# Performance work log

Measured on AMD Instinct MI355X. Metric: run time of the kernel, lower is better.

The kernel has to match this reference:

```python
import jax, jax.numpy as jnp
import numpy as np

B, S, H, NH, HD = 2, 1024, 1024, 16, 64
L, C, E, K, D = 256, 2048, 8, 2, 2048
EPS = 1e-5


def _ln(x):
    m = x.mean(-1, keepdims=True)
    v = x.var(-1, keepdims=True)
    return (x - m) * jax.lax.rsqrt(v + EPS)


def _rot_half(x):
    h = x.shape[-1] // 2
    return jnp.concatenate([-x[..., h:], x[..., :h]], axis=-1)


def _attn(q, k, v, scale):
    s = jnp.einsum('bhqd,bhkd->bhqk', q, k) * scale
    p = jax.nn.softmax(s, axis=-1)
    return jnp.einsum('bhqk,bhkd->bhqd', p, v)


def _forward(x, condition, enc, rope_cos, rope_sin, adaln_w, adaln_b, qw, qb, kw, kb, vw, vb, ow, ob, cqw, cqb, ckw, ckb, cvw, cvb, cow, cob, cn_g, cn_b, gate_w, ew1, eb1, ew2, eb2):
    b, s, hdim = x.shape
    # AdaLN-Zero modulation params (condition is per-sample vector)
    mod = jax.nn.silu(condition) @ adaln_w + adaln_b
    sh1, sc1, g1, sh2, sc2, g2 = jnp.split(mod, 6, axis=-1)
    # --- self-attention with RoPE ---
    h = _ln(x) * (1 + sc1[:, None]) + sh1[:, None]
    q = (h @ qw + qb).reshape(b, s, NH, HD).transpose(0, 2, 1, 3)
    k = (h @ kw + kb).reshape(b, s, NH, HD).transpose(0, 2, 1, 3)
    v = (h @ vw + vb).reshape(b, s, NH, HD).transpose(0, 2, 1, 3)
    cos = rope_cos[None, None]
    sin = rope_sin[None, None]
    q = q * cos + _rot_half(q) * sin
    k = k * cos + _rot_half(k) * sin
    a = _attn(q, k, v, 1.0 / np.sqrt(HD)).transpose(0, 2, 1, 3).reshape(b, s, hdim)
    x = x + g1[:, None] * (a @ ow + ob)
    # --- cross-attention (affine LayerNorm) ---
    hc = _ln(x) * cn_g + cn_b
    lq = (hc @ cqw + cqb).reshape(b, s, NH, HD).transpose(0, 2, 1, 3)
    lk = (enc @ ckw + ckb).reshape(b, -1, NH, HD).transpose(0, 2, 1, 3)
    lv = (enc @ cvw + cvb).reshape(b, -1, NH, HD).transpose(0, 2, 1, 3)
    ca = _attn(lq, lk, lv, 1.0 / np.sqrt(HD)).transpose(0, 2, 1, 3).reshape(b, s, hdim)
    x = x + ca @ cow + cob
    # --- MoE FFN with AdaLN-Zero modulation ---
    h = _ln(x) * (1 + sc2[:, None]) + sh2[:, None]
    logits = h @ gate_w                                   # [B,S,E]
    probs = jax.nn.softmax(logits, axis=-1)
    topp, topi = jax.lax.top_k(probs, K)                  # [B,S,K]
    topp = topp / topp.sum(-1, keepdims=True)
    onehot = jax.nn.one_hot(topi, E, dtype=x.dtype)       # [B,S,K,E]
    cw = (onehot * topp[..., None]).sum(-2)               # [B,S,E] combine weights
    tokens_per_expert = onehot.sum(-2).mean(0)            # [S,E] (matches torch one_hot(...).sum(-2).mean(0))
    avg_prob = probs.mean((0, 1))                         # [E]
    aux = E * (tokens_per_expert * avg_prob).sum()
    hf = h.reshape(-1, hdim)                              # [T,H]
    act = jax.nn.gelu(jnp.einsum('th,ehd->ted', hf, ew1) + eb1, approximate=False)
    y = jnp.einsum('ted,edh->teh', act, ew2) + eb2        # [T,E,H]
    moe = jnp.einsum('te,teh->th', cw.reshape(-1, E), y).reshape(b, s, hdim)
    x = x + g2[:, None] * moe
    return x, aux


def setup_inputs() -> dict:
    key = jax.random.key(0)
    ks = jax.random.split(key, 30)
    w = lambda i, shape: (jax.random.normal(ks[i], shape) * 0.02).astype(jnp.float32)
    pos = jnp.arange(S, dtype=jnp.float32)[:, None]
    inv = 1.0 / (10000.0 ** (jnp.arange(0, HD, 2, dtype=jnp.float32) / HD))
    ang = jnp.concatenate([pos * inv[None, :]] * 2, axis=-1)  # [S,HD]
    return dict(
        x=jax.random.normal(ks[0], (B, S, H), jnp.float32),
        condition=jax.random.normal(ks[1], (B, H), jnp.float32),
        enc=jax.random.normal(ks[2], (B, L, C), jnp.float32),
        rope_cos=jnp.cos(ang).astype(jnp.float32),
        rope_sin=jnp.sin(ang).astype(jnp.float32),
        adaln_w=w(3, (H, 6 * H)), adaln_b=w(4, (6 * H,)),
        qw=w(5, (H, H)), qb=w(6, (H,)), kw=w(7, (H, H)), kb=w(8, (H,)),
        vw=w(9, (H, H)), vb=w(10, (H,)), ow=w(11, (H, H)), ob=w(12, (H,)),
        cqw=w(13, (H, H)), cqb=w(14, (H,)), ckw=w(15, (C, H)), ckb=w(16, (H,)),
        cvw=w(17, (C, H)), cvb=w(18, (H,)), cow=w(19, (H, H)), cob=w(20, (H,)),
        cn_g=jnp.ones((H,), jnp.float32), cn_b=jnp.zeros((H,), jnp.float32),
        gate_w=w(21, (H, E)),
        ew1=w(22, (E, H, D)), eb1=w(23, (E, D)),
        ew2=w(24, (E, D, H)), eb2=w(25, (E, H)),
    )


def reference(x, condition, enc, rope_cos, rope_sin, adaln_w, adaln_b, qw, qb, kw, kb, vw, vb, ow, ob, cqw, cqb, ckw, ckb, cvw, cvb, cow, cob, cn_g, cn_b, gate_w, ew1, eb1, ew2, eb2):
    return _forward(x, condition, enc, rope_cos, rope_sin, adaln_w, adaln_b, qw, qb, kw, kb, vw, vb, ow, ob, cqw, cqb, ckw, ckb, cvw, cvb, cow, cob, cn_g, cn_b, gate_w, ew1, eb1, ew2, eb2)
```

## Files before the change

### kernel.cpp

```cpp
#include <hip/hip_runtime.h>
#include <math.h>

#define Hh 1024
#define Ss 1024
#define Bb 2
#define NHh 16
#define HDd 64
#define Tt 2048
#define Ll 256
#define Cc 2048
#define Ee 8
#define Dd 2048
#define EPSf 1e-5f
#define PADROWS 5120

using bf16x8 = __attribute__((ext_vector_type(8))) short;
using f32x4  = __attribute__((ext_vector_type(4))) float;
using ushort8 = __attribute__((ext_vector_type(8))) unsigned short;

__device__ __forceinline__ float geluf(float x) {
    return 0.5f * x * (1.0f + erff(x * 0.70710678118654752f));
}

__device__ __forceinline__ unsigned short f2bf(float x) {
    union { float f; unsigned int u; } c; c.f = x;
    unsigned int r = (c.u + 0x7fffu + ((c.u >> 16) & 1u)) >> 16;
    return (unsigned short)r;
}

__device__ __forceinline__ void gload16(const void* g, void* l) {
    __builtin_amdgcn_global_load_lds(
        (const __attribute__((address_space(1))) void*)g,
        (__attribute__((address_space(3))) void*)l, 16, 0, 0);
}

__device__ __forceinline__ void tcast_tile(const float* __restrict__ src,
        unsigned short* __restrict__ dst, int R, int C, int lt,
        unsigned short* __restrict__ tb, int tid) {
    int gx = R >> 7;
    int rt = lt % gx, ct = lt / gx;
    int r0 = rt * 128, c0 = ct * 64;
    int lr = tid >> 4;
    int lc4 = (tid & 15) << 2;
    #pragma unroll
    for (int p = 0; p < 8; ++p) {
        int row = lr + 16 * p;
        float4 v = *(const float4*)&src[(size_t)(r0 + row) * C + c0 + lc4];
        ushort4 h; h.x = f2bf(v.x); h.y = f2bf(v.y); h.z = f2bf(v.z); h.w = f2bf(v.w);
        *(ushort4*)&tb[row * 70 + lc4] = h;
    }
    __syncthreads();
    int wr = tid >> 5;
    int wc4 = (tid & 31) << 2;
    #pragma unroll
    for (int p = 0; p < 8; ++p) {
        int orow = wr + 8 * p;
        ushort4 o;
        o.x = tb[(wc4 + 0) * 70 + orow];
        o.y = tb[(wc4 + 1) * 70 + orow];
        o.z = tb[(wc4 + 2) * 70 + orow];
        o.w = tb[(wc4 + 3) * 70 + orow];
        *(ushort4*)&dst[(size_t)(c0 + orow) * R + r0 + wc4] = o;
    }
}

__global__ __launch_bounds__(256) void prep_all(
        const float* __restrict__ qw, const float* __restrict__ kw, const float* __restrict__ vw,
        const float* __restrict__ ow, const float* __restrict__ cqw, const float* __restrict__ cow,
        const float* __restrict__ ckw, const float* __restrict__ cvw,
        const float* __restrict__ enc,
        const float* __restrict__ qb, const float* __restrict__ kb, const float* __restrict__ vb,
        const float* __restrict__ ckb, const float* __restrict__ cvb,
        unsigned short* __restrict__ qkvwT, unsigned short* __restrict__ owT,
        unsigned short* __restrict__ cqwT, unsigned short* __restrict__ cowT,
        unsigned short* __restrict__ ckvwT, unsigned short* __restrict__ encb,
        float* __restrict__ qkvb, float* __restrict__ ckvb) {
    __shared__ unsigned short tb[128 * 70];
    int bid = blockIdx.x;
    int tid = threadIdx.x;
    const float* src;
    unsigned short* dst;
    int R, C, lt;
    if (bid < 768) {
        int seg = bid >> 7;
        lt = bid & 127;
        R = 1024; C = 1024;
        switch (seg) {
            case 0: src = qw;  dst = qkvwT; break;
            case 1: src = kw;  dst = qkvwT + (size_t)1024 * 1024; break;
            case 2: src = vw;  dst = qkvwT + (size_t)2048 * 1024; break;
            case 3: src = ow;  dst = owT; break;
            case 4: src = cqw; dst = cqwT; break;
            default: src = cow; dst = cowT; break;
        }
    } else if (bid < 1024) {
        lt = bid - 768; src = ckw; dst = ckvwT; R = 2048; C = 1024;
    } else if (bid < 1280) {
        lt = bid - 1024; src = cvw; dst = ckvwT + (size_t)1024 * 2048; R = 2048; C = 1024;
    } else if (bid < 2304) {
        int i = (bid - 1280) * 256 + tid;
        float4 v = ((const float4*)enc)[i];
        ushort4 o; o.x = f2bf(v.x); o.y = f2bf(v.y); o.z = f2bf(v.z); o.w = f2bf(v.w);
        ((ushort4*)encb)[i] = o;
        return;
    } else {
        int i = (bid - 2304) * 256 + tid;
        if (i < 1024) qkvb[i] = qb[i];
        else if (i < 2048) qkvb[i] = kb[i - 1024];
        else if (i < 3072) qkvb[i] = vb[i - 2048];
        else if (i < 4096) ckvb[i - 3072] = ckb[i - 3072];
        else if (i < 5120) ckvb[i - 3072] = cvb[i - 4096];
        return;
    }
    tcast_tile(src, dst, R, C, lt, tb, tid);
}

__global__ __launch_bounds__(256) void vtrans16(const unsigned short* __restrict__ in,
        unsigned short* __restrict__ out, int S) {
    __shared__ unsigned short sm[32][36];
    int bh = blockIdx.z;
    int s0 = blockIdx.x * 32, d0 = blockIdx.y * 32;
    int lr = threadIdx.x >> 3, lc = (threadIdx.x & 7) << 2;
    ushort4 v = *(const ushort4*)&in[((size_t)bh * S + s0 + lr) * 64 + d0 + lc];
    sm[lr][lc] = v.x; sm[lr][lc + 1] = v.y; sm[lr][lc + 2] = v.z; sm[lr][lc + 3] = v.w;
    __syncthreads();
    ushort4 o;
    o.x = sm[lc + 0][lr]; o.y = sm[lc + 1][lr]; o.z = sm[lc + 2][lr]; o.w = sm[lc + 3][lr];
    *(ushort4*)&out[((size_t)bh * 64 + d0 + lr) * S + s0 + lc] = o;
}

__global__ __launch_bounds__(256) void adaln_kernel(const float* __restrict__ cond,
        const float* __restrict__ w, const float* __restrict__ b, float* __restrict__ mod) {
    __shared__ float ss[Hh];
    int bi = (blockIdx.x * 256) / (6 * Hh);
    const float* cp = cond + (size_t)bi * Hh;
    for (int i = threadIdx.x; i < Hh; i += 256) {
        float c = cp[i];
        ss[i] = c / (1.0f + expf(-c));
    }
    __syncthreads();
    int idx = blockIdx.x * 256 + threadIdx.x;
    int j = idx % (6 * Hh);
    float acc = b[j];
    for (int i = 0; i < Hh; ++i) acc += ss[i] * w[(size_t)i * (6 * Hh) + j];
    mod[idx] = acc;
}

template<int OM>
__global__ __launch_bounds__(256) void ln_affine(const float* __restrict__ X, float* __restrict__ O32,
        unsigned short* __restrict__ O16,
        const float* __restrict__ scale, const float* __restrict__ shift, int bstride, float add1) {
    int t = blockIdx.x;
    int tid = threadIdx.x;
    const float* xr = X + (size_t)t * Hh;
    float4 xv = *(const float4*)&xr[tid * 4];
    float s = xv.x + xv.y + xv.z + xv.w;
    float q = xv.x * xv.x + xv.y * xv.y + xv.z * xv.z + xv.w * xv.w;
    #pragma unroll
    for (int off = 32; off > 0; off >>= 1) {
        s += __shfl_down(s, off);
        q += __shfl_down(q, off);
    }
    __shared__ float rsum[4], rsq[4];
    __shared__ float smean, srstd;
    int wv = tid >> 6, ln = tid & 63;
    if (ln == 0) { rsum[wv] = s; rsq[wv] = q; }
    __syncthreads();
    if (tid == 0) {
        float ts = rsum[0] + rsum[1] + rsum[2] + rsum[3];
        float tq = rsq[0] + rsq[1] + rsq[2] + rsq[3];
        float mean = ts * (1.0f / Hh);
        float var = tq * (1.0f / Hh) - mean * mean;
        smean = mean; srstd = rsqrtf(var + EPSf);
    }
    __syncthreads();
    float mean = smean, rstd = srstd;
    int bi = t >> 10;
    int j = tid * 4;
    const float* scp = scale + (size_t)bi * bstride;
    const float* shp = shift + (size_t)bi * bstride;
    float4 sc4 = *(const float4*)&scp[j];
    float4 sh4 = *(const float4*)&shp[j];
    float4 o;
    o.x = (xv.x - mean) * rstd * (add1 + sc4.x) + sh4.x;
    o.y = (xv.y - mean) * rstd * (add1 + sc4.y) + sh4.y;
    o.z = (xv.z - mean) * rstd * (add1 + sc4.z) + sh4.z;
    o.w = (xv.w - mean) * rstd * (add1 + sc4.w) + sh4.w;
    if (OM & 1) *(float4*)&O32[(size_t)t * Hh + j] = o;
    if (OM & 2) {
        ushort4 h; h.x = f2bf(o.x); h.y = f2bf(o.y); h.z = f2bf(o.z); h.w = f2bf(o.w);
        *(ushort4*)&O16[(size_t)t * Hh + j] = h;
    }
}

__global__ __launch_bounds__(512) void gemm_qkv(const unsigned short* __restrict__ A,
        const unsigned short* __restrict__ Bt, const float* __restrict__ bias,
        unsigned short* __restrict__ P0, unsigned short* __restrict__ P1,
        unsigned short* __restrict__ P2, const float* __restrict__ rc, const float* __restrict__ rsn,
        int K) {
    __shared__ unsigned short As[2][128 * 32];
    __shared__ unsigned short Bs[2][128 * 32];
    int m0 = blockIdx.x * 128, n0 = blockIdx.y * 128;
    int tid = threadIdx.x;
    int lane = tid & 63;
    int wv = tid >> 6;
    int wm = (wv >> 1) * 32, wn = (wv & 1) * 64;
    f32x4 acc[2][4] = {};
    int r0 = tid >> 2, q8 = (tid & 3) * 8;
    const unsigned short* gA = A + (size_t)(m0 + r0) * K + q8;
    const unsigned short* gB = Bt + (size_t)(n0 + r0) * K + q8;
    int ra = (lane & 15) * 32 + (lane >> 4) * 8;
    auto stage = [&](int kk, int bufi) {
        gload16(gA + kk, &As[bufi][tid * 8]);
        gload16(gB + kk, &Bs[bufi][tid * 8]);
    };
    int nsteps = K / 32;
    stage(0, 0);
    int cur = 0;
    for (int s = 0; s < nsteps; ++s) {
        if (s + 1 < nsteps) {
            stage((s + 1) * 32, cur ^ 1);
            asm volatile("s_waitcnt vmcnt(2)" ::: "memory");
        } else {
            asm volatile("s_waitcnt vmcnt(0)" ::: "memory");
        }
        __builtin_amdgcn_s_barrier();
        bf16x8 af[2], bf[4];
        #pragma unroll
        for (int f = 0; f < 2; ++f) af[f] = *(const bf16x8*)&As[cur][(wm + f * 16) * 32 + ra];
        #pragma unroll
        for (int f = 0; f < 4; ++f) bf[f] = *(const bf16x8*)&Bs[cur][(wn + f * 16) * 32 + ra];
        #pragma unroll
        for (int i = 0; i < 2; ++i)
            #pragma unroll
            for (int j = 0; j < 4; ++j)
                acc[i][j] = __builtin_amdgcn_mfma_f32_16x16x32_bf16(af[i], bf[j], acc[i][j], 0, 0, 0);
        asm volatile("s_waitcnt lgkmcnt(0)" ::: "memory");
        __builtin_amdgcn_s_barrier();
        cur ^= 1;
    }
    int colb = n0 + wn + (lane & 15);
    int rowb = m0 + wm + (lane >> 4) * 4;
    float bv[4];
    #pragma unroll
    for (int j = 0; j < 4; ++j) bv[j] = bias[colb + j * 16];
    int nh = (colb >> 6) & 15;
    int type = colb >> 10;
    float qs = (type == 0) ? 0.125f : 1.0f;
    #pragma unroll
    for (int i = 0; i < 2; ++i) {
        #pragma unroll
        for (int r = 0; r < 4; ++r) {
            int row = rowb + i * 16 + r;
            int b = row >> 10, s = row & 1023;
            unsigned short* dst = (type == 0) ? P0 : (type == 1 ? P1 : P2);
            size_t obase = ((size_t)((b * 16 + nh) * 1024 + s)) * 64;
            if (type < 2) {
                #pragma unroll
                for (int j = 0; j < 2; ++j) {
                    int hd = j * 16 + (lane & 15);
                    float v0 = acc[i][j][r] + bv[j];
                    float v2 = acc[i][j + 2][r] + bv[j + 2];
                    float c1 = rc[s * 64 + hd], s1 = rsn[s * 64 + hd];
                    float c2 = rc[s * 64 + hd + 32], s2 = rsn[s * 64 + hd + 32];
                    dst[obase + hd] = f2bf((v0 * c1 - v2 * s1) * qs);
                    dst[obase + hd + 32] = f2bf((v2 * c2 + v0 * s2) * qs);
                }
            } else {
                #pragma unroll
                for (int j = 0; j < 4; ++j)
                    dst[obase + j * 16 + (lane & 15)] = f2bf(acc[i][j][r] + bv[j]);
            }
        }
    }
}

template<int EP>
__global__ __launch_bounds__(256) void gemm64(const unsigned short* __restrict__ A,
        const unsigned short* __restrict__ Bt, const float* __restrict__ bias,
        float* __restrict__ Cf, unsigned short* __restrict__ P0, unsigned short* __restrict__ P1,
        const float* __restrict__ baseb, const float* __restrict__ gatep,
        int M, int N, int K) {
    __shared__ unsigned short As[2][64 * 32];
    __shared__ unsigned short Bs[2][64 * 32];
    int m0 = blockIdx.x * 64, n0 = blockIdx.y * 64;
    int tid = threadIdx.x;
    int lane = tid & 63;
    int wv = tid >> 6;
    int wm = (wv >> 1) * 32, wn = (wv & 1) * 32;
    f32x4 acc[2][2] = {};
    int r0 = tid >> 2, q8 = (tid & 3) * 8;
    const unsigned short* gA = A + (size_t)(m0 + r0) * K + q8;
    const unsigned short* gB = Bt + (size_t)(n0 + r0) * K + q8;
    int ra = (lane & 15) * 32 + (lane >> 4) * 8;
    auto stage = [&](int kk, int bufi) {
        gload16(gA + kk, &As[bufi][tid * 8]);
        gload16(gB + kk, &Bs[bufi][tid * 8]);
    };
    int nsteps = K / 32;
    stage(0, 0);
    int cur = 0;
    for (int s = 0; s < nsteps; ++s) {
        if (s + 1 < nsteps) {
            stage((s + 1) * 32, cur ^ 1);
            asm volatile("s_waitcnt vmcnt(2)" ::: "memory");
        } else {
            asm volatile("s_waitcnt vmcnt(0)" ::: "memory");
        }
        __builtin_amdgcn_s_barrier();
        bf16x8 af[2], bf[2];
        #pragma unroll
        for (int f = 0; f < 2; ++f) {
            af[f] = *(const bf16x8*)&As[cur][(wm + f * 16) * 32 + ra];
            bf[f] = *(const bf16x8*)&Bs[cur][(wn + f * 16) * 32 + ra];
        }
        #pragma unroll
        for (int i = 0; i < 2; ++i)
            #pragma unroll
            for (int j = 0; j < 2; ++j)
                acc[i][j] = __builtin_amdgcn_mfma_f32_16x16x32_bf16(af[i], bf[j], acc[i][j], 0, 0, 0);
        asm volatile("s_waitcnt lgkmcnt(0)" ::: "memory");
        __builtin_amdgcn_s_barrier();
        cur ^= 1;
    }
    int colb = n0 + wn + (lane & 15);
    int rowb = m0 + wm + (lane >> 4) * 4;
    float bv[2];
    #pragma unroll
    for (int j = 0; j < 2; ++j) bv[j] = bias[colb + j * 16];
    if (EP == 0 || EP == 4 || EP == 5) {
        #pragma unroll
        for (int j = 0; j < 2; ++j) {
            int col = colb + j * 16;
            #pragma unroll
            for (int i = 0; i < 2; ++i)
                #pragma unroll
                for (int r = 0; r < 4; ++r) {
                    int row = rowb + i * 16 + r;
                    size_t gi = (size_t)row * N + col;
                    float v = acc[i][j][r] + bv[j];
                    if (EP == 0) {
                        Cf[gi] = v;
                    } else if (EP == 4) {
                        float g = gatep[(row >> 10) * (6 * Hh) + col];
                        Cf[gi] = baseb[gi] + g * v;
                    } else {
                        Cf[gi] = baseb[gi] + v;
                    }
                }
        }
        return;
    }
    int nh = (colb >> 6) & 15;
    int type = colb >> 10;
    int hd0 = colb & 63;
    #pragma unroll
    for (int i = 0; i < 2; ++i) {
        #pragma unroll
        for (int r = 0; r < 4; ++r) {
            int row = rowb + i * 16 + r;
            if (EP == 2) {
                int b = row >> 8, s = row & 255;
                unsigned short* dst = (type == 0) ? P0 : P1;
                size_t obase = ((size_t)((b * 16 + nh) * 256 + s)) * 64;
                #pragma unroll
                for (int j = 0; j < 2; ++j)
                    dst[obase + hd0 + j * 16] = f2bf(acc[i][j][r] + bv[j]);
            } else {
                int b = row >> 10, s = row & 1023;
                size_t obase = ((size_t)((b * 16 + nh) * 1024 + s)) * 64;
                #pragma unroll
                for (int j = 0; j < 2; ++j)
                    P0[obase + hd0 + j * 16] = f2bf((acc[i][j][r] + bv[j]) * 0.125f);
            }
        }
    }
}

__global__ __launch_bounds__(512) void gemm_moe1(const unsigned short* __restrict__ A,
        const unsigned short* __restrict__ W, const float* __restrict__ bias,
        unsigned short* __restrict__ Og, const int* __restrict__ cnt,
        const int* __restrict__ offp, const int* __restrict__ gtok) {
    __shared__ unsigned short As[2][128 * 32];
    __shared__ unsigned short Bs[2][128 * 32];
    int m0 = blockIdx.x * 128;
    if (m0 >= offp[Ee]) return;
    int e = 0;
    while (offp[e + 1] <= m0) ++e;
    int base = offp[e], valid = cnt[e];
    int n0 = blockIdx.y * 128;
    int tid = threadIdx.x;
    int lane = tid & 63;
    int wv = tid >> 6;
    int wm = (wv >> 1) * 32, wn = (wv & 1) * 64;
    f32x4 acc[2][4] = {};
    int r0 = tid >> 2, q8 = (tid & 3) * 8;
    int lr0 = m0 - base + r0;
    int tok0 = gtok[base + (lr0 < valid ? lr0 : 0)];
    const unsigned short* gA = A + (size_t)tok0 * Hh + q8;
    const unsigned short* Wt = W + (size_t)e * Dd * Hh;
    const unsigned short* gB = Wt + (size_t)(n0 + r0) * Hh + q8;
    int ra = (lane & 15) * 32 + (lane >> 4) * 8;
    auto stage = [&](int kk, int bufi) {
        gload16(gA + kk, &As[bufi][tid * 8]);
        gload16(gB + kk, &Bs[bufi][tid * 8]);
    };
    int nsteps = Hh / 32;
    stage(0, 0);
    int cur = 0;
    for (int s = 0; s < nsteps; ++s) {
        if (s + 1 < nsteps) {
            stage((s + 1) * 32, cur ^ 1);
            asm volatile("s_waitcnt vmcnt(2)" ::: "memory");
        } else {
            asm volatile("s_waitcnt vmcnt(0)" ::: "memory");
        }
        __builtin_amdgcn_s_barrier();
        bf16x8 af[2], bf[4];
        #pragma unroll
        for (int f = 0; f < 2; ++f) af[f] = *(const bf16x8*)&As[cur][(wm + f * 16) * 32 + ra];
        #pragma unroll
        for (int f = 0; f < 4; ++f) bf[f] = *(const bf16x8*)&Bs[cur][(wn + f * 16) * 32 + ra];
        #pragma unroll
        for (int i = 0; i < 2; ++i)
            #pragma unroll
            for (int j = 0; j < 4; ++j)
                acc[i][j] = __builtin_amdgcn_mfma_f32_16x16x32_bf16(af[i], bf[j], acc[i][j], 0, 0, 0);
        asm volatile("s_waitcnt lgkmcnt(0)" ::: "memory");
        __builtin_amdgcn_s_barrier();
        cur ^= 1;
    }
    int colb = n0 + wn + (lane & 15);
    int rowtb = wm + (lane >> 4) * 4;
    const float* bp = bias + (size_t)e * Dd;
    #pragma unroll
    for (int j = 0; j < 4; ++j) {
        int col = colb + j * 16;
        float bv = bp[col];
        #pragma unroll
        for (int i = 0; i < 2; ++i) {
            #pragma unroll
            for (int r = 0; r < 4; ++r) {
                int rt = rowtb + i * 16 + r;
                if (m0 - base + rt < valid)
                    Og[(size_t)(m0 + rt) * Dd + col] = f2bf(geluf(acc[i][j][r] + bv));
            }
        }
    }
}

__global__ __launch_bounds__(512) void gemm_moe2(const unsigned short* __restrict__ A,
        const unsigned short* __restrict__ W, const float* __restrict__ bias,
        float* __restrict__ outp, const int* __restrict__ cnt,
        const int* __restrict__ offp, const int* __restrict__ gtok, const float* __restrict__ gwt,
        const float* __restrict__ gate2) {
    __shared__ unsigned short As[2][128 * 32];
    __shared__ unsigned short Bs[2][128 * 32];
    int m0 = blockIdx.x * 128;
    if (m0 >= offp[Ee]) return;
    int e = 0;
    while (offp[e + 1] <= m0) ++e;
    int base = offp[e], valid = cnt[e];
    int n0 = blockIdx.y * 128;
    int tid = threadIdx.x;
    int lane = tid & 63;
    int wv = tid >> 6;
    int wm = (wv >> 1) * 32, wn = (wv & 1) * 64;
    f32x4 acc[2][4] = {};
    int r0 = tid >> 2, q8 = (tid & 3) * 8;
    const unsigned short* gA = A + (size_t)(m0 + r0) * Dd + q8;
    const unsigned short* Wt = W + (size_t)e * Hh * Dd;
    const unsigned short* gB = Wt + (size_t)(n0 + r0) * Dd + q8;
    int ra = (lane & 15) * 32 + (lane >> 4) * 8;
    auto stage = [&](int kk, int bufi) {
        gload16(gA + kk, &As[bufi][tid * 8]);
        gload16(gB + kk, &Bs[bufi][tid * 8]);
    };
    int nsteps = Dd / 32;
    stage(0, 0);
    int cur = 0;
    for (int s = 0; s < nsteps; ++s) {
        if (s + 1 < nsteps) {
            stage((s + 1) * 32, cur ^ 1);
            asm volatile("s_waitcnt vmcnt(2)" ::: "memory");
        } else {
            asm volatile("s_waitcnt vmcnt(0)" ::: "memory");
        }
        __builtin_amdgcn_s_barrier();
        bf16x8 af[2], bf[4];
        #pragma unroll
        for (int f = 0; f < 2; ++f) af[f] = *(const bf16x8*)&As[cur][(wm + f * 16) * 32 + ra];
        #pragma unroll
        for (int f = 0; f < 4; ++f) bf[f] = *(const bf16x8*)&Bs[cur][(wn + f * 16) * 32 + ra];
        #pragma unroll
        for (int i = 0; i < 2; ++i)
            #pragma unroll
            for (int j = 0; j < 4; ++j)
                acc[i][j] = __builtin_amdgcn_mfma_f32_16x16x32_bf16(af[i], bf[j], acc[i][j], 0, 0, 0);
        asm volatile("s_waitcnt lgkmcnt(0)" ::: "memory");
        __builtin_amdgcn_s_barrier();
        cur ^= 1;
    }
    int colb = n0 + wn + (lane & 15);
    int rowtb = wm + (lane >> 4) * 4;
    const float* bp = bias + (size_t)e * Hh;
    #pragma unroll
    for (int j = 0; j < 4; ++j) {
        int col = colb + j * 16;
        float bv = bp[col];
        float g2a = gate2[col];
        float g2b = gate2[6 * Hh + col];
        #pragma unroll
        for (int i = 0; i < 2; ++i) {
            #pragma unroll
            for (int r = 0; r < 4; ++r) {
                int rt = rowtb + i * 16 + r;
                int g = m0 + rt;
                if (g - base < valid) {
                    float w = gwt[g];
                    int tok = gtok[g];
                    float g2 = (tok >> 10) ? g2b : g2a;
                    atomicAdd(&outp[(size_t)tok * Hh + col], g2 * w * (acc[i][j][r] + bv));
                }
            }
        }
    }
}

__global__ __launch_bounds__(256) void fattn_m(const unsigned short* __restrict__ Qp,
        const unsigned short* __restrict__ Kp, const unsigned short* __restrict__ Vtp,
        unsigned short* __restrict__ O, int Skv,
        const float* __restrict__ ew1, const float* __restrict__ ew2,
        unsigned short* __restrict__ ew1T, unsigned short* __restrict__ ew2T) {
    __shared__ unsigned short shbuf[4 * 64 * 72];
    int tid = threadIdx.x;
    if (blockIdx.y >= 32) {
        int tile = blockIdx.x + 16 * (blockIdx.y - 32);
        if (tile < 2048) {
            int e = tile >> 8, lt = tile & 255;
            tcast_tile(ew1 + (size_t)e * 1024 * 2048, ew1T + (size_t)e * 2048 * 1024,
                       1024, 2048, lt, shbuf, tid);
        } else {
            int t2 = tile - 2048;
            int e = t2 >> 8, lt = t2 & 255;
            tcast_tile(ew2 + (size_t)e * 2048 * 1024, ew2T + (size_t)e * 1024 * 2048,
                       2048, 1024, lt, shbuf, tid);
        }
        return;
    }
    unsigned short* Qs  = shbuf;
    unsigned short* Ks  = shbuf + 64 * 72;
    unsigned short* Vts = shbuf + 2 * 64 * 72;
    unsigned short* Ps  = shbuf + 3 * 64 * 72;
    int q0 = blockIdx.x * 64;
    int bh = blockIdx.y;
    int b = bh >> 4, nh = bh & 15;
    int lane = tid & 63, w = tid >> 6;
    int sr = tid >> 2, sp = (tid & 3) * 16;
    {
        const unsigned short* src = &Qp[((size_t)bh * 1024 + q0 + sr) * 64 + sp];
        *(ushort8*)&Qs[sr * 72 + sp] = *(const ushort8*)&src[0];
        *(ushort8*)&Qs[sr * 72 + sp + 8] = *(const ushort8*)&src[8];
    }
    f32x4 acc[4] = {};
    float m_old[4], l_run[4];
    #pragma unroll
    for (int r = 0; r < 4; ++r) { m_old[r] = -1e30f; l_run[r] = 0.0f; }
    int wrow = w * 16;
    int k8 = (lane >> 4) * 8;
    ushort8 pkA, pkB, pvA, pvB;
    {
        const unsigned short* ksrc = &Kp[((size_t)bh * Skv + sr) * 64 + sp];
        pkA = *(const ushort8*)&ksrc[0];
        pkB = *(const ushort8*)&ksrc[8];
        const unsigned short* vsrc = &Vtp[((size_t)bh * 64 + sr) * Skv + sp];
        pvA = *(const ushort8*)&vsrc[0];
        pvB = *(const ushort8*)&vsrc[8];
    }
    for (int k0 = 0; k0 < Skv; k0 += 64) {
        asm volatile("s_waitcnt lgkmcnt(0)" ::: "memory");
        __builtin_amdgcn_s_barrier();
        *(ushort8*)&Ks[sr * 72 + sp] = pkA;
        *(ushort8*)&Ks[sr * 72 + sp + 8] = pkB;
        *(ushort8*)&Vts[sr * 72 + sp] = pvA;
        *(ushort8*)&Vts[sr * 72 + sp + 8] = pvB;
        if (k0 + 64 < Skv) {
            const unsigned short* ksrc = &Kp[((size_t)bh * Skv + k0 + 64 + sr) * 64 + sp];
            pkA = *(const ushort8*)&ksrc[0];
            pkB = *(const ushort8*)&ksrc[8];
            const unsigned short* vsrc = &Vtp[((size_t)bh * 64 + sr) * Skv + k0 + 64 + sp];
            pvA = *(const ushort8*)&vsrc[0];
            pvB = *(const ushort8*)&vsrc[8];
        }
        asm volatile("s_waitcnt lgkmcnt(0)" ::: "memory");
        __builtin_amdgcn_s_barrier();
        bf16x8 aq0 = *(const bf16x8*)&Qs[(wrow + (lane & 15)) * 72 + k8];
        bf16x8 aq1 = *(const bf16x8*)&Qs[(wrow + (lane & 15)) * 72 + 32 + k8];
        f32x4 sf[4];
        __builtin_amdgcn_s_setprio(1);
        #pragma unroll
        for (int j = 0; j < 4; ++j) {
            bf16x8 bk0 = *(const bf16x8*)&Ks[(j * 16 + (lane & 15)) * 72 + k8];
            bf16x8 bk1 = *(const bf16x8*)&Ks[(j * 16 + (lane & 15)) * 72 + 32 + k8];
            f32x4 z = {};
            z = __builtin_amdgcn_mfma_f32_16x16x32_bf16(aq0, bk0, z, 0, 0, 0);
            z = __builtin_amdgcn_mfma_f32_16x16x32_bf16(aq1, bk1, z, 0, 0, 0);
            sf[j] = z;
        }
        __builtin_amdgcn_s_setprio(0);
        float p[4][4];
        float fsc[4];
        #pragma unroll
        for (int r = 0; r < 4; ++r) {
            float mx = fmaxf(fmaxf(sf[0][r], sf[1][r]), fmaxf(sf[2][r], sf[3][r]));
            #pragma unroll
            for (int mk = 1; mk < 16; mk <<= 1) mx = fmaxf(mx, __shfl_xor(mx, mk));
            float mn = fmaxf(m_old[r], mx);
            float f = __expf(m_old[r] - mn);
            float rs = 0.0f;
            #pragma unroll
            for (int j = 0; j < 4; ++j) {
                p[j][r] = __expf(sf[j][r] - mn);
                rs += p[j][r];
            }
            #pragma unroll
            for (int mk = 1; mk < 16; mk <<= 1) rs += __shfl_xor(rs, mk);
            l_run[r] = l_run[r] * f + rs;
            m_old[r] = mn;
            fsc[r] = f;
        }
        #pragma unroll
        for (int jd = 0; jd < 4; ++jd)
            #pragma unroll
            for (int r = 0; r < 4; ++r) acc[jd][r] *= fsc[r];
        #pragma unroll
        for (int j = 0; j < 4; ++j)
            #pragma unroll
            for (int r = 0; r < 4; ++r)
                Ps[(wrow + (lane >> 4) * 4 + r) * 72 + j * 16 + (lane & 15)] = f2bf(p[j][r]);
        asm volatile("s_waitcnt lgkmcnt(0)" ::: "memory");
        __builtin_amdgcn_s_barrier();
        bf16x8 ap0 = *(const bf16x8*)&Ps[(wrow + (lane & 15)) * 72 + k8];
        bf16x8 ap1 = *(const bf16x8*)&Ps[(wrow + (lane & 15)) * 72 + 32 + k8];
        __builtin_amdgcn_s_setprio(1);
        #pragma unroll
        for (int jd = 0; jd < 4; ++jd) {
            bf16x8 bv0 = *(const bf16x8*)&Vts[(jd * 16 + (lane & 15)) * 72 + k8];
            bf16x8 bv1 = *(const bf16x8*)&Vts[(jd * 16 + (lane & 15)) * 72 + 32 + k8];
            acc[jd] = __builtin_amdgcn_mfma_f32_16x16x32_bf16(ap0, bv0, acc[jd], 0, 0, 0);
            acc[jd] = __builtin_amdgcn_mfma_f32_16x16x32_bf16(ap1, bv1, acc[jd], 0, 0, 0);
        }
        __builtin_amdgcn_s_setprio(0);
    }
    float inv[4];
    #pragma unroll
    for (int r = 0; r < 4; ++r) inv[r] = 1.0f / l_run[r];
    #pragma unroll
    for (int jd = 0; jd < 4; ++jd)
        #pragma unroll
        for (int r = 0; r < 4; ++r)
            O[((size_t)(b * Ss + q0 + wrow + (lane >> 4) * 4 + r)) * Hh + nh * 64 + jd * 16 + (lane & 15)]
                = f2bf(acc[jd][r] * inv[r]);
}

__global__ __launch_bounds__(256) void gate_kernel(const float* __restrict__ h,
        const float* __restrict__ gw, float* __restrict__ probs, int* __restrict__ topi,
        float* __restrict__ topw) {
    int t = blockIdx.x * 4 + (threadIdx.x >> 6);
    int lane = threadIdx.x & 63;
    const float* hp = h + (size_t)t * Hh;
    float lg[Ee] = {};
    #pragma unroll
    for (int s = 0; s < 4; ++s) {
        int d0 = s * 256 + lane * 4;
        float4 hv = *(const float4*)&hp[d0];
        float hv4[4] = {hv.x, hv.y, hv.z, hv.w};
        #pragma unroll
        for (int c = 0; c < 4; ++c) {
            float hx = hv4[c];
            const float* g0 = &gw[(size_t)(d0 + c) * Ee];
            #pragma unroll
            for (int e = 0; e < Ee; ++e) lg[e] += hx * g0[e];
        }
    }
    #pragma unroll
    for (int e = 0; e < Ee; ++e)
        #pragma unroll
        for (int mk = 1; mk < 64; mk <<= 1) lg[e] += __shfl_xor(lg[e], mk);
    if (lane == 0) {
        float m = lg[0];
        #pragma unroll
        for (int e = 1; e < Ee; ++e) m = fmaxf(m, lg[e]);
        float ssum = 0;
        #pragma unroll
        for (int e = 0; e < Ee; ++e) { lg[e] = expf(lg[e] - m); ssum += lg[e]; }
        float inv = 1.0f / ssum;
        #pragma unroll
        for (int e = 0; e < Ee; ++e) { lg[e] *= inv; probs[t * Ee + e] = lg[e]; }
        int i0 = 0;
        #pragma unroll
        for (int e = 1; e < Ee; ++e) if (lg[e] > lg[i0]) i0 = e;
        int i1 = (i0 == 0) ? 1 : 0;
        #pragma unroll
        for (int e = 0; e < Ee; ++e) if (e != i1 && e != i0 && lg[e] > lg[i1]) i1 = e;
        float w0 = lg[i0], w1 = lg[i1];
        float inv2 = 1.0f / (w0 + w1);
        topi[t * 2] = i0; topi[t * 2 + 1] = i1;
        topw[t * 2] = w0 * inv2; topw[t * 2 + 1] = w1 * inv2;
    }
}

__global__ __launch_bounds__(1024) void moe_prep(const float* __restrict__ probs,
        const int* __restrict__ topi, const float* __restrict__ topw,
        int* __restrict__ cnt, int* __restrict__ offp,
        int* __restrict__ gtok, float* __restrict__ gwt, float* __restrict__ auxout) {
    __shared__ int scnt[Ee], spos[Ee], soff[Ee + 1];
    __shared__ float sS[Ee], sC[Ee];
    int tid = threadIdx.x;
    if (tid < Ee) { scnt[tid] = 0; spos[tid] = 0; sS[tid] = 0.0f; sC[tid] = 0.0f; }
    __syncthreads();
    float lp[Ee] = {};
    float lc[Ee] = {};
    for (int t = tid; t < Tt; t += 1024) {
        int a0 = topi[2 * t], a1 = topi[2 * t + 1];
        atomicAdd(&scnt[a0], 1);
        atomicAdd(&scnt[a1], 1);
        #pragma unroll
        for (int e = 0; e < Ee; ++e) lp[e] += probs[t * Ee + e];
        lc[a0] += 1.0f; lc[a1] += 1.0f;
    }
    #pragma unroll
    for (int e = 0; e < Ee; ++e) {
        atomicAdd(&sS[e], lp[e]);
        atomicAdd(&sC[e], lc[e]);
    }
    __syncthreads();
    if (tid == 0) {
        int acc = 0;
        for (int e = 0; e < Ee; ++e) { soff[e] = acc; acc += (scnt[e] + 127) & ~127; }
        soff[Ee] = acc;
        float aux = 0.0f;
        for (int e = 0; e < Ee; ++e) aux += sS[e] * sC[e];
        auxout[0] = aux * (8.0f / 4096.0f);
    }
    if (tid < Ee) cnt[tid] = scnt[tid];
    __syncthreads();
    if (tid <= Ee) offp[tid] = soff[tid];
    for (int t = tid; t < Tt; t += 1024) {
        #pragma unroll
        for (int s = 0; s < 2; ++s) {
            int e = topi[2 * t + s];
            int pos = atomicAdd(&spos[e], 1);
            int g = soff[e] + pos;
            gtok[g] = t;
            gwt[g] = topw[2 * t + s];
        }
    }
}

extern "C" void kernel_launch(void* const* d_in, const int* in_sizes, int n_in,
                              void* d_out, int out_size, void* d_ws, size_t ws_size,
                              hipStream_t stream) {
    (void)in_sizes; (void)n_in; (void)out_size; (void)ws_size;
    const float* x    = (const float*)d_in[0];
    const float* cond = (const float*)d_in[1];
    const float* enc  = (const float*)d_in[2];
    const float* rc   = (const float*)d_in[3];
    const float* rsn  = (const float*)d_in[4];
    const float* adw  = (const float*)d_in[5];
    const float* adb  = (const float*)d_in[6];
    const float* qw  = (const float*)d_in[7];  const float* qb  = (const float*)d_in[8];
    const float* kw  = (const float*)d_in[9];  const float* kb2 = (const float*)d_in[10];
    const float* vw  = (const float*)d_in[11]; const float* vb  = (const float*)d_in[12];
    const float* ow  = (const float*)d_in[13]; const float* ob  = (const float*)d_in[14];
    const float* cqw = (const float*)d_in[15]; const float* cqb = (const float*)d_in[16];
    const float* ckw = (const float*)d_in[17]; const float* ckb = (const float*)d_in[18];
    const float* cvw = (const float*)d_in[19]; const float* cvb = (const float*)d_in[20];
    const float* cow = (const float*)d_in[21]; const float* cob = (const float*)d_in[22];
    const float* cng = (const float*)d_in[23]; const float* cnb = (const float*)d_in[24];
    const float* gatew = (const float*)d_in[25];
    const float* ew1 = (const float*)d_in[26]; const float* eb1 = (const float*)d_in[27];
    const float* ew2 = (const float*)d_in[28]; const float* eb2 = (const float*)d_in[29];
    float* out = (float*)d_out;

    char* ws = (char*)d_ws;
    size_t off = 0;
    auto alloc = [&](size_t bytes) {
        char* p = ws + off;
        off += (bytes + 255) & ~(size_t)255;
        return (void*)p;
    };
    float* hbuf   = (float*)alloc((size_t)Tt * Hh * 4);
    float* mod    = (float*)alloc((size_t)Bb * 6 * Hh * 4);
    float* probs  = (float*)alloc((size_t)Tt * Ee * 4);
    float* topw   = (float*)alloc((size_t)Tt * 2 * 4);
    int*   topi   = (int*)alloc((size_t)Tt * 2 * 4);
    float* qkvb   = (float*)alloc(3072 * 4);
    float* ckvb   = (float*)alloc(2048 * 4);
    int*   cntbuf = (int*)alloc(16 * 4);
    int*   offp   = (int*)alloc(16 * 4);
    int*   gtok   = (int*)alloc((size_t)PADROWS * 4);
    float* gwt    = (float*)alloc((size_t)PADROWS * 4);
    typedef unsigned short u16;
    u16* h1b   = (u16*)alloc((size_t)Tt * Hh * 2);
    u16* hcb   = (u16*)alloc((size_t)Tt * Hh * 2);
    u16* h2b   = (u16*)alloc((size_t)Tt * Hh * 2);
    u16* abb   = (u16*)alloc((size_t)Tt * Hh * 2);
    u16* encb  = (u16*)alloc((size_t)Bb * Ll * Cc * 2);
    u16* actg  = (u16*)alloc((size_t)PADROWS * Dd * 2);
    u16* Qb16  = (u16*)alloc((size_t)32 * 1024 * 64 * 2);
    u16* Kb16  = (u16*)alloc((size_t)32 * 1024 * 64 * 2);
    u16* Vb16  = (u16*)alloc((size_t)32 * 1024 * 64 * 2);
    u16* Vt16  = (u16*)alloc((size_t)32 * 64 * 1024 * 2);
    u16* cQ16  = (u16*)alloc((size_t)32 * 1024 * 64 * 2);
    u16* cK16  = (u16*)alloc((size_t)32 * 256 * 64 * 2);
    u16* cV16  = (u16*)alloc((size_t)32 * 256 * 64 * 2);
    u16* cVt16 = (u16*)alloc((size_t)32 * 64 * 256 * 2);
    u16* qkvwT = (u16*)alloc((size_t)3072 * 1024 * 2);
    u16* owT   = (u16*)alloc((size_t)1024 * 1024 * 2);
    u16* cqwT  = (u16*)alloc((size_t)1024 * 1024 * 2);
    u16* ckvwT = (u16*)alloc((size_t)2048 * 2048 * 2);
    u16* cowT  = (u16*)alloc((size_t)1024 * 1024 * 2);
    u16* ew1T  = (u16*)alloc((size_t)Ee * Hh * Dd * 2);
    u16* ew2T  = (u16*)alloc((size_t)Ee * Dd * Hh * 2);

    dim3 blk(256);
    dim3 blk512(512);
    prep_all<<<dim3(2324), blk, 0, stream>>>(qw, kw, vw, ow, cqw, cow, ckw, cvw, enc,
        qb, kb2, vb, ckb, cvb, qkvwT, owT, cqwT, cowT, ckvwT, encb, qkvb, ckvb);
    adaln_kernel<<<dim3(Bb * 6 * Hh / 256), blk, 0, stream>>>(cond, adw, adb, mod);
    ln_affine<2><<<dim3(Tt), blk, 0, stream>>>(x, nullptr, h1b, mod + Hh, mod + 0, 6 * Hh, 1.0f);
    gemm_qkv<<<dim3(Tt / 128, 3072 / 128), blk512, 0, stream>>>(h1b, qkvwT, qkvb,
        Qb16, Kb16, Vb16, rc, rsn, 1024);
    vtrans16<<<dim3(32, 2, 32), blk, 0, stream>>>(Vb16, Vt16, 1024);
    fattn_m<<<dim3(16, 32 + 256), blk, 0, stream>>>(Qb16, Kb16, Vt16, abb, 1024,
        ew1, ew2, ew1T, ew2T);
    gemm64<4><<<dim3(Tt / 64, Hh / 64), blk, 0, stream>>>(abb, owT, ob, out,
        nullptr, nullptr, x, mod + 2 * Hh, Tt, Hh, 1024);
    ln_affine<2><<<dim3(Tt), blk, 0, stream>>>(out, nullptr, hcb, cng, cnb, 0, 0.0f);
    gemm64<3><<<dim3(Tt / 64, Hh / 64), blk, 0, stream>>>(hcb, cqwT, cqb, nullptr,
        cQ16, nullptr, nullptr, nullptr, Tt, Hh, 1024);
    gemm64<2><<<dim3(Bb * Ll / 64, 2048 / 64), blk, 0, stream>>>(encb, ckvwT, ckvb, nullptr,
        cK16, cV16, nullptr, nullptr, Bb * Ll, 2048, Cc);
    vtrans16<<<dim3(8, 2, 32), blk, 0, stream>>>(cV16, cVt16, 256);
    fattn_m<<<dim3(16, 32), blk, 0, stream>>>(cQ16, cK16, cVt16, abb, 256,
        ew1, ew2, ew1T, ew2T);
    gemm64<5><<<dim3(Tt / 64, Hh / 64), blk, 0, stream>>>(abb, cowT, cob, out,
        nullptr, nullptr, out, nullptr, Tt, Hh, 1024);
    ln_affine<3><<<dim3(Tt), blk, 0, stream>>>(out, hbuf, h2b, mod + 4 * Hh, mod + 3 * Hh, 6 * Hh, 1.0f);
    gate_kernel<<<dim3(Tt / 4), blk, 0, stream>>>(hbuf, gatew, probs, topi, topw);
    moe_prep<<<dim3(1), dim3(1024), 0, stream>>>(probs, topi, topw, cntbuf, offp, gtok, gwt,
        out + (size_t)Tt * Hh);
    gemm_moe1<<<dim3(PADROWS / 128, Dd / 128), blk512, 0, stream>>>(h2b, ew1T, eb1, actg, cntbuf, offp, gtok);
    gemm_moe2<<<dim3(PADROWS / 128, Hh / 128), blk512, 0, stream>>>(actg, ew2T, eb2, out, cntbuf, offp, gtok, gwt,
        mod + 5 * Hh);
}
```

Measured before the change: 417.3 us.

## Move non-QKV weight transposes and enc cast into the QKV GEMM launch

The prep kernel now only transposes the Q/K/V weights and copies biases. The remaining weight transposes (ow, cqw, cow, ckw, cvw) and the enc bf16 cast run as extra blocks appended to the QKV GEMM grid, using a 512-thread tile variant and the GEMM's shared buffer. This shortens the serial prep phase ahead of the QKV GEMM and overlaps the conversion work with GEMM blocks. The cost is a larger GEMM grid with mixed block types, which may affect scheduling.

```diff
diff --git a/kernel.cpp b/kernel.cpp
--- a/kernel.cpp
+++ b/kernel.cpp
@@ -64,55 +64,58 @@
     }
 }
 
+__device__ __forceinline__ void tcast_tile512(const float* __restrict__ src,
+        unsigned short* __restrict__ dst, int R, int C, int lt,
+        unsigned short* __restrict__ tb, int tid) {
+    int gx = R >> 7;
+    int rt = lt % gx, ct = lt / gx;
+    int r0 = rt * 128, c0 = ct * 64;
+    int lr = tid >> 4;
+    int lc4 = (tid & 15) << 2;
+    #pragma unroll
+    for (int p = 0; p < 4; ++p) {
+        int row = lr + 32 * p;
+        float4 v = *(const float4*)&src[(size_t)(r0 + row) * C + c0 + lc4];
+        ushort4 h; h.x = f2bf(v.x); h.y = f2bf(v.y); h.z = f2bf(v.z); h.w = f2bf(v.w);
+        *(ushort4*)&tb[row * 70 + lc4] = h;
+    }
+    __syncthreads();
+    int wr = tid >> 5;
+    int wc4 = (tid & 31) << 2;
+    #pragma unroll
+    for (int p = 0; p < 4; ++p) {
+        int orow = wr + 16 * p;
+        ushort4 o;
+        o.x = tb[(wc4 + 0) * 70 + orow];
+        o.y = tb[(wc4 + 1) * 70 + orow];
+        o.z = tb[(wc4 + 2) * 70 + orow];
+        o.w = tb[(wc4 + 3) * 70 + orow];
+        *(ushort4*)&dst[(size_t)(c0 + orow) * R + r0 + wc4] = o;
+    }
+}
+
 __global__ __launch_bounds__(256) void prep_all(
         const float* __restrict__ qw, const float* __restrict__ kw, const float* __restrict__ vw,
-        const float* __restrict__ ow, const float* __restrict__ cqw, const float* __restrict__ cow,
-        const float* __restrict__ ckw, const float* __restrict__ cvw,
-        const float* __restrict__ enc,
         const float* __restrict__ qb, const float* __restrict__ kb, const float* __restrict__ vb,
         const float* __restrict__ ckb, const float* __restrict__ cvb,
-        unsigned short* __restrict__ qkvwT, unsigned short* __restrict__ owT,
-        unsigned short* __restrict__ cqwT, unsigned short* __restrict__ cowT,
-        unsigned short* __restrict__ ckvwT, unsigned short* __restrict__ encb,
-        float* __restrict__ qkvb, float* __restrict__ ckvb) {
+        unsigned short* __restrict__ qkvwT, float* __restrict__ qkvb, float* __restrict__ ckvb) {
     __shared__ unsigned short tb[128 * 70];
     int bid = blockIdx.x;
     int tid = threadIdx.x;
-    const float* src;
-    unsigned short* dst;
-    int R, C, lt;
-    if (bid < 768) {
+    if (bid < 384) {
         int seg = bid >> 7;
-        lt = bid & 127;
-        R = 1024; C = 1024;
-        switch (seg) {
-            case 0: src = qw;  dst = qkvwT; break;
-            case 1: src = kw;  dst = qkvwT + (size_t)1024 * 1024; break;
-            case 2: src = vw;  dst = qkvwT + (size_t)2048 * 1024; break;
-            case 3: src = ow;  dst = owT; break;
-            case 4: src = cqw; dst = cqwT; break;
-            default: src = cow; dst = cowT; break;
-        }
-    } else if (bid < 1024) {
-        lt = bid - 768; src = ckw; dst = ckvwT; R = 2048; C = 1024;
-    } else if (bid < 1280) {
-        lt = bid - 1024; src = cvw; dst = ckvwT + (size_t)1024 * 2048; R = 2048; C = 1024;
-    } else if (bid < 2304) {
-        int i = (bid - 1280) * 256 + tid;
-        float4 v = ((const float4*)enc)[i];
-        ushort4 o; o.x = f2bf(v.x); o.y = f2bf(v.y); o.z = f2bf(v.z); o.w = f2bf(v.w);
-        ((ushort4*)encb)[i] = o;
+        int lt = bid & 127;
+        const float* src = (seg == 0) ? qw : (seg == 1 ? kw : vw);
+        unsigned short* dst = qkvwT + (size_t)seg * 1024 * 1024;
+        tcast_tile(src, dst, 1024, 1024, lt, tb, tid);
         return;
-    } else {
-        int i = (bid - 2304) * 256 + tid;
-        if (i < 1024) qkvb[i] = qb[i];
-        else if (i < 2048) qkvb[i] = kb[i - 1024];
-        else if (i < 3072) qkvb[i] = vb[i - 2048];
-        else if (i < 4096) ckvb[i - 3072] = ckb[i - 3072];
-        else if (i < 5120) ckvb[i - 3072] = cvb[i - 4096];
-        return;
-    }
-    tcast_tile(src, dst, R, C, lt, tb, tid);
+    }
+    int i = (bid - 384) * 256 + tid;
+    if (i < 1024) qkvb[i] = qb[i];
+    else if (i < 2048) qkvb[i] = kb[i - 1024];
+    else if (i < 3072) qkvb[i] = vb[i - 2048];
+    else if (i < 4096) ckvb[i - 3072] = ckb[i - 3072];
+    else if (i < 5120) ckvb[i - 3072] = cvb[i - 4096];
 }
 
 __global__ __launch_bounds__(256) void vtrans16(const unsigned short* __restrict__ in,
@@ -197,11 +200,36 @@
         const unsigned short* __restrict__ Bt, const float* __restrict__ bias,
         unsigned short* __restrict__ P0, unsigned short* __restrict__ P1,
         unsigned short* __restrict__ P2, const float* __restrict__ rc, const float* __restrict__ rsn,
-        int K) {
-    __shared__ unsigned short As[2][128 * 32];
-    __shared__ unsigned short Bs[2][128 * 32];
+        const float* __restrict__ ow, const float* __restrict__ cqw, const float* __restrict__ cow,
+        const float* __restrict__ ckw, const float* __restrict__ cvw, const float* __restrict__ enc,
+        unsigned short* __restrict__ owT, unsigned short* __restrict__ cqwT,
+        unsigned short* __restrict__ cowT, unsigned short* __restrict__ ckvwT,
+        unsigned short* __restrict__ encb, int K) {
+    __shared__ unsigned short sh[2 * 128 * 32 * 2];
+    int tid = threadIdx.x;
+    if (blockIdx.y >= 24) {
+        int t = blockIdx.x + 16 * (blockIdx.y - 24);
+        if (t < 384) {
+            int seg = t >> 7, lt = t & 127;
+            const float* src = (seg == 0) ? ow : (seg == 1 ? cqw : cow);
+            unsigned short* dst = (seg == 0) ? owT : (seg == 1 ? cqwT : cowT);
+            tcast_tile512(src, dst, 1024, 1024, lt, sh, tid);
+        } else if (t < 896) {
+            int t2 = t - 384;
+            const float* src = (t2 < 256) ? ckw : cvw;
+            unsigned short* dst = (t2 < 256) ? ckvwT : (ckvwT + (size_t)1024 * 2048);
+            tcast_tile512(src, dst, 2048, 1024, t2 & 255, sh, tid);
+        } else {
+            int i = (t - 896) * 512 + tid;
+            float4 v = ((const float4*)enc)[i];
+            ushort4 o; o.x = f2bf(v.x); o.y = f2bf(v.y); o.z = f2bf(v.z); o.w = f2bf(v.w);
+            ((ushort4*)encb)[i] = o;
+        }
+        return;
+    }
+    unsigned short* As0 = sh;
+    unsigned short* Bs0 = sh + 2 * 128 * 32;
     int m0 = blockIdx.x * 128, n0 = blockIdx.y * 128;
-    int tid = threadIdx.x;
     int lane = tid & 63;
     int wv = tid >> 6;
     int wm = (wv >> 1) * 32, wn = (wv & 1) * 64;
@@ -211,8 +239,8 @@
     const unsigned short* gB = Bt + (size_t)(n0 + r0) * K + q8;
     int ra = (lane & 15) * 32 + (lane >> 4) * 8;
     auto stage = [&](int kk, int bufi) {
-        gload16(gA + kk, &As[bufi][tid * 8]);
-        gload16(gB + kk, &Bs[bufi][tid * 8]);
+        gload16(gA + kk, &As0[bufi * 128 * 32 + tid * 8]);
+        gload16(gB + kk, &Bs0[bufi * 128 * 32 + tid * 8]);
     };
     int nsteps = K / 32;
     stage(0, 0);
@@ -227,9 +255,9 @@
         __builtin_amdgcn_s_barrier();
         bf16x8 af[2], bf[4];
         #pragma unroll
-        for (int f = 0; f < 2; ++f) af[f] = *(const bf16x8*)&As[cur][(wm + f * 16) * 32 + ra];
-        #pragma unroll
-        for (int f = 0; f < 4; ++f) bf[f] = *(const bf16x8*)&Bs[cur][(wn + f * 16) * 32 + ra];
+        for (int f = 0; f < 2; ++f) af[f] = *(const bf16x8*)&As0[cur * 128 * 32 + (wm + f * 16) * 32 + ra];
+        #pragma unroll
+        for (int f = 0; f < 4; ++f) bf[f] = *(const bf16x8*)&Bs0[cur * 128 * 32 + (wn + f * 16) * 32 + ra];
         #pragma unroll
         for (int i = 0; i < 2; ++i)
             #pragma unroll
@@ -826,12 +854,13 @@
 
     dim3 blk(256);
     dim3 blk512(512);
-    prep_all<<<dim3(2324), blk, 0, stream>>>(qw, kw, vw, ow, cqw, cow, ckw, cvw, enc,
-        qb, kb2, vb, ckb, cvb, qkvwT, owT, cqwT, cowT, ckvwT, encb, qkvb, ckvb);
+    prep_all<<<dim3(404), blk, 0, stream>>>(qw, kw, vw, qb, kb2, vb, ckb, cvb,
+        qkvwT, qkvb, ckvb);
     adaln_kernel<<<dim3(Bb * 6 * Hh / 256), blk, 0, stream>>>(cond, adw, adb, mod);
     ln_affine<2><<<dim3(Tt), blk, 0, stream>>>(x, nullptr, h1b, mod + Hh, mod + 0, 6 * Hh, 1.0f);
-    gemm_qkv<<<dim3(Tt / 128, 3072 / 128), blk512, 0, stream>>>(h1b, qkvwT, qkvb,
-        Qb16, Kb16, Vb16, rc, rsn, 1024);
+    gemm_qkv<<<dim3(16, 24 + 88), blk512, 0, stream>>>(h1b, qkvwT, qkvb,
+        Qb16, Kb16, Vb16, rc, rsn,
+        ow, cqw, cow, ckw, cvw, enc, owT, cqwT, cowT, ckvwT, encb, 1024);
     vtrans16<<<dim3(32, 2, 32), blk, 0, stream>>>(Vb16, Vt16, 1024);
     fattn_m<<<dim3(16, 32 + 256), blk, 0, stream>>>(Qb16, Kb16, Vt16, abb, 1024,
         ew1, ew2, ew1T, ew2T);
```

Result: faster. 408.9 us (-2.0%).
